# Kernel optimization log

Hardware: AMD Instinct MI355X
Metric: run time of the kernel (lower is better)

The kernel has to match this reference:

```python
import jax, jax.numpy as jnp
import numpy as np

N, Wt, Tt, DIM = 16, 256, 2048, 256
EPS = 1e-5

def silu(x):
    return x * jax.nn.sigmoid(x)

def setup_inputs() -> dict:
    key = jax.random.key(0)
    ks = jax.random.split(key, 12)
    d = {}
    d['T'] = jnp.arange(Tt, dtype=jnp.float32)
    d['durations'] = jax.random.uniform(ks[0], (N, Wt, 1), jnp.float32)
    d['features'] = jax.random.normal(ks[1], (N, Wt, DIM), jnp.float32)
    d['conv1_w'] = jax.random.normal(ks[2], (8, DIM, 3), jnp.float32) * 0.05
    d['conv1_b'] = jnp.zeros((8,), jnp.float32)
    d['bn1_g'] = jnp.ones((8,), jnp.float32)
    d['bn1_b'] = jnp.zeros((8,), jnp.float32)
    d['bn1_m'] = jnp.zeros((8,), jnp.float32)
    d['bn1_v'] = jnp.ones((8,), jnp.float32)
    d['conv2_w'] = jax.random.normal(ks[3], (8, DIM, 3), jnp.float32) * 0.05
    d['conv2_b'] = jnp.zeros((8,), jnp.float32)
    d['bn2_g'] = jnp.ones((8,), jnp.float32)
    d['bn2_b'] = jnp.zeros((8,), jnp.float32)
    d['bn2_m'] = jnp.zeros((8,), jnp.float32)
    d['bn2_v'] = jnp.ones((8,), jnp.float32)
    d['sb1_w1'] = jax.random.normal(ks[4], (10, 2), jnp.float32) * 0.3
    d['sb1_b1'] = jnp.zeros((2,), jnp.float32)
    d['sb1_w2'] = jax.random.normal(ks[5], (2, 2), jnp.float32) * 0.3
    d['sb1_b2'] = jnp.zeros((2,), jnp.float32)
    d['sb2_w1'] = jax.random.normal(ks[6], (10, 16), jnp.float32) * 0.3
    d['sb2_b1'] = jnp.zeros((16,), jnp.float32)
    d['sb2_w2'] = jax.random.normal(ks[7], (16, 16), jnp.float32) * 0.3
    d['sb2_b2'] = jnp.zeros((16,), jnp.float32)
    d['proj1_w'] = jax.random.normal(ks[8], (2, DIM), jnp.float32) * 0.3
    d['proj1_b'] = jnp.zeros((DIM,), jnp.float32)
    d['proj2_w'] = jax.random.normal(ks[9], (16, 1), jnp.float32) * 0.3
    d['proj2_b'] = jnp.zeros((1,), jnp.float32)
    return d

def _conv_bn_silu(x_ncw, w, b, g, beta, m, v):
    # Conv1d(dim->8, k=3, pad=1) + BatchNorm(eval) + SiLU
    y = jax.lax.conv_general_dilated(x_ncw, w, (1,), [(1, 1)],
                                     dimension_numbers=('NCH', 'OIH', 'NCH'))
    y = y + b[None, :, None]
    y = (y - m[None, :, None]) * jax.lax.rsqrt(v[None, :, None] + EPS)
    y = y * g[None, :, None] + beta[None, :, None]
    return silu(y)

def _swish_block(x, w1, b1, w2, b2):
    x = silu(x @ w1 + b1)
    return silu(x @ w2 + b2)

def reference(T, durations, features, conv1_w, conv1_b, bn1_g, bn1_b, bn1_m, bn1_v,
              conv2_w, conv2_b, bn2_g, bn2_b, bn2_m, bn2_v,
              sb1_w1, sb1_b1, sb1_w2, sb1_b2, sb2_w1, sb2_b1, sb2_w2, sb2_b2,
              proj1_w, proj1_b, proj2_w, proj2_b):
    feat = jnp.swapaxes(features, 1, 2)  # (N, C, W)
    n, _, w = feat.shape
    t = T.shape[0]
    left = jnp.swapaxes(_conv_bn_silu(feat, conv1_w, conv1_b, bn1_g, bn1_b, bn1_m, bn1_v), 1, 2)   # (N, W, 8)
    right = jnp.swapaxes(_conv_bn_silu(feat, conv2_w, conv2_b, bn2_g, bn2_b, bn2_m, bn2_v), 1, 2)  # (N, W, 8)
    token_end = jnp.cumsum(durations, axis=1)        # (N, W, 1)
    token_start = token_end - durations              # (N, W, 1)
    S = T[None, None, :] - token_start               # (N, W, T)
    E = token_end - T[None, None, :]                 # (N, W, T)
    left_b = jnp.broadcast_to(left[:, :, None, :], (n, w, t, 8))
    right_b = jnp.broadcast_to(right[:, :, None, :], (n, w, t, 8))
    xleft = jnp.concatenate([S[..., None], E[..., None], left_b], axis=-1)    # (N, W, T, 10)
    xright = jnp.concatenate([S[..., None], E[..., None], right_b], axis=-1)  # (N, W, T, 10)
    C = _swish_block(xleft, sb1_w1, sb1_b1, sb1_w2, sb1_b2)                   # (N, W, T, 2)
    xr = _swish_block(xright, sb2_w1, sb2_b1, sb2_w2, sb2_b2)                 # (N, W, T, 16)
    score = (xr @ proj2_w + proj2_b)[..., 0]                                  # (N, W, T)
    Wsm = jax.nn.softmax(score, axis=1)  # softmax over tokens W
    out_r = jnp.einsum('nkt,ndk->ntd', Wsm, feat)                             # (N, T, dim)
    out_l = jnp.einsum('nkt,nktp->ntp', Wsm, C) @ proj1_w + proj1_b           # (N, T, dim)
    return out_l + out_r
```

## Files before the change

kernel.cpp:

```cpp
#include <hip/hip_runtime.h>
#include <hip/hip_bf16.h>

#define NN  16
#define WT  256
#define TT  2048
#define DIM 256
#define TBT 8

typedef __attribute__((ext_vector_type(8))) short short8_t;
typedef __attribute__((ext_vector_type(4))) float f32x4;

__device__ __forceinline__ float fast_rcp(float x){ return __builtin_amdgcn_rcpf(x); }

__device__ __forceinline__ float silu_f(float x){
    return x * fast_rcp(1.0f + __expf(-x));
}

__device__ __forceinline__ unsigned short f2bf(float x){
    union { float f; unsigned u; } v; v.f = x;
    unsigned r = v.u + 0x7FFFu + ((v.u >> 16) & 1u);
    return (unsigned short)(r >> 16);
}

__device__ __forceinline__ void fma4(float4& a, float s, const float4& f){
    a.x = fmaf(s, f.x, a.x); a.y = fmaf(s, f.y, a.y);
    a.z = fmaf(s, f.z, a.z); a.w = fmaf(s, f.w, a.w);
}

__global__ __launch_bounds__(256) void prep_k(
    const float* __restrict__ dur, const float* __restrict__ feat,
    const float* __restrict__ c1w, const float* __restrict__ c1b,
    const float* __restrict__ g1,  const float* __restrict__ be1,
    const float* __restrict__ m1,  const float* __restrict__ vv1,
    const float* __restrict__ c2w, const float* __restrict__ c2b,
    const float* __restrict__ g2,  const float* __restrict__ be2,
    const float* __restrict__ m2,  const float* __restrict__ vv2,
    const float* __restrict__ sb1w1, const float* __restrict__ sb1b1,
    const float* __restrict__ sb2w1, const float* __restrict__ sb2b1,
    float* __restrict__ v1o, float* __restrict__ v2o)
{
    int w = blockIdx.x, n = blockIdx.y;
    int tid = threadIdx.x;

    __shared__ float sdur[WT];
    sdur[tid] = dur[n*WT + tid];
    __syncthreads();
    for (int off = 1; off < WT; off <<= 1){
        float v = (tid >= off) ? sdur[tid-off] : 0.0f;
        __syncthreads();
        sdur[tid] += v;
        __syncthreads();
    }
    float end   = sdur[w];
    float start = end - dur[n*WT + w];

    const float* fb = feat + (size_t)(n*WT)*DIM;
    float fm = (w > 0)    ? fb[(size_t)(w-1)*DIM + tid] : 0.0f;
    float f0 =              fb[(size_t) w   *DIM + tid];
    float fp = (w < WT-1) ? fb[(size_t)(w+1)*DIM + tid] : 0.0f;

    float pl[8], pr[8];
    #pragma unroll
    for (int o = 0; o < 8; o++){
        const float* wp = c1w + (size_t)(o*DIM + tid)*3;
        pl[o] = fmaf(fm, wp[0], fmaf(f0, wp[1], fp*wp[2]));
        const float* wq = c2w + (size_t)(o*DIM + tid)*3;
        pr[o] = fmaf(fm, wq[0], fmaf(f0, wq[1], fp*wq[2]));
    }
    #pragma unroll
    for (int o = 0; o < 8; o++){
        #pragma unroll
        for (int off = 32; off; off >>= 1){
            pl[o] += __shfl_xor(pl[o], off);
            pr[o] += __shfl_xor(pr[o], off);
        }
    }
    __shared__ float sws[4][16];
    int wave = tid >> 6, lane = tid & 63;
    if (lane == 0){
        #pragma unroll
        for (int o = 0; o < 8; o++){ sws[wave][o] = pl[o]; sws[wave][8+o] = pr[o]; }
    }
    __syncthreads();
    __shared__ float slr[16];
    if (tid < 16){
        float s = sws[0][tid] + sws[1][tid] + sws[2][tid] + sws[3][tid];
        int o = tid & 7; bool isr = tid >= 8;
        float bias = isr ? c2b[o] : c1b[o];
        float mm   = isr ? m2[o]  : m1[o];
        float vv   = isr ? vv2[o] : vv1[o];
        float gg   = isr ? g2[o]  : g1[o];
        float bb   = isr ? be2[o] : be1[o];
        float y = s + bias;
        y = (y - mm) * rsqrtf(vv + 1e-5f);
        y = y * gg + bb;
        slr[tid] = silu_f(y);
    }
    __syncthreads();
    if (tid < 16){
        int j = tid;
        float acc = sb2b1[j] - start*sb2w1[j] + end*sb2w1[16 + j];
        #pragma unroll
        for (int o = 0; o < 8; o++) acc = fmaf(slr[8+o], sb2w1[(2+o)*16 + j], acc);
        v2o[(size_t)(n*WT + w)*16 + j] = acc;
    } else if (tid < 18){
        int p = tid - 16;
        float acc = sb1b1[p] - start*sb1w1[p] + end*sb1w1[2 + p];
        #pragma unroll
        for (int o = 0; o < 8; o++) acc = fmaf(slr[o], sb1w1[(2+o)*2 + p], acc);
        v1o[(size_t)(n*WT + w)*2 + p] = acc;
    }
}

__global__ __launch_bounds__(256) void featpack_k(const float* __restrict__ feat,
                                                  unsigned short* __restrict__ featP)
{
    int kb = blockIdx.x, n = blockIdx.y;
    int d = threadIdx.x;
    const float* fb = feat + (size_t)n*WT*DIM + (size_t)kb*32*DIM + d;
    unsigned short* op = featP + ((size_t)(n*8 + kb)*DIM + d)*32;
    unsigned short buf[32];
    #pragma unroll
    for (int e = 0; e < 32; e++) buf[e] = f2bf(fb[(size_t)e*DIM]);
    #pragma unroll
    for (int g = 0; g < 4; g++){
        uint4 u;
        u.x = (unsigned)buf[g*8+0] | ((unsigned)buf[g*8+1] << 16);
        u.y = (unsigned)buf[g*8+2] | ((unsigned)buf[g*8+3] << 16);
        u.z = (unsigned)buf[g*8+4] | ((unsigned)buf[g*8+5] << 16);
        u.w = (unsigned)buf[g*8+6] | ((unsigned)buf[g*8+7] << 16);
        *(uint4*)(op + g*8) = u;
    }
}

__global__ __launch_bounds__(256) void score_k(
    const float* __restrict__ Tg,
    const float* __restrict__ v1g, const float* __restrict__ v2g,
    const float* __restrict__ sb1w1, const float* __restrict__ sb1w2, const float* __restrict__ sb1b2,
    const float* __restrict__ sb2w1, const float* __restrict__ sb2w2, const float* __restrict__ sb2b2,
    const float* __restrict__ p2w, const float* __restrict__ p2b,
    unsigned short* __restrict__ wsm_b, float* __restrict__ wc_g)
{
    int n   = blockIdx.y;
    int t0  = blockIdx.x * TBT;
    int tid = threadIdx.x;
    int w   = tid;
    int lane = tid & 63, wave = tid >> 6;

    __shared__ float s_w2[16*16];
    __shared__ float s_u2[16], s_b2[16], s_p2w[16];
    __shared__ float s_u1[2], s_w21[4], s_b21[2];
    __shared__ float s_xa[4][TBT];
    __shared__ float s_xs[4][TBT];
    __shared__ float s_xc0[4][TBT], s_xc1[4][TBT];

    s_w2[tid] = sb2w2[tid];
    if (tid < 16){
        s_u2[tid]  = sb2w1[tid] - sb2w1[16 + tid];
        s_b2[tid]  = sb2b2[tid];
        s_p2w[tid] = p2w[tid];
    } else if (tid < 18){
        int p = tid - 16;
        s_u1[p]  = sb1w1[p] - sb1w1[2 + p];
        s_b21[p] = sb1b2[p];
    } else if (tid < 22){
        s_w21[tid - 18] = sb1w2[tid - 18];
    }
    __syncthreads();

    float v2r[16];
    {
        const float4* vp = (const float4*)(v2g + (size_t)(n*WT + w)*16);
        float4 a = vp[0], b = vp[1], c = vp[2], d = vp[3];
        v2r[0]=a.x; v2r[1]=a.y; v2r[2]=a.z; v2r[3]=a.w;
        v2r[4]=b.x; v2r[5]=b.y; v2r[6]=b.z; v2r[7]=b.w;
        v2r[8]=c.x; v2r[9]=c.y; v2r[10]=c.z; v2r[11]=c.w;
        v2r[12]=d.x; v2r[13]=d.y; v2r[14]=d.z; v2r[15]=d.w;
    }
    float v1r0, v1r1;
    {
        const float* vp = v1g + (size_t)(n*WT + w)*2;
        v1r0 = vp[0]; v1r1 = vp[1];
    }
    float p2bv = p2b[0];
    float tv[TBT];
    #pragma unroll
    for (int ti = 0; ti < TBT; ti++) tv[ti] = Tg[t0 + ti];

    float scores[TBT];
    #pragma unroll
    for (int tp = 0; tp < TBT; tp += 2){
        float h2a[16], h2b[16];
        #pragma unroll
        for (int j = 0; j < 16; j++){ float b = s_b2[j]; h2a[j] = b; h2b[j] = b; }
        #pragma unroll
        for (int i = 0; i < 16; i++){
            float u = s_u2[i], v = v2r[i];
            float aa = silu_f(fmaf(tv[tp],   u, v));
            float ab = silu_f(fmaf(tv[tp+1], u, v));
            #pragma unroll
            for (int j = 0; j < 16; j++){
                float wv = s_w2[i*16 + j];
                h2a[j] = fmaf(aa, wv, h2a[j]);
                h2b[j] = fmaf(ab, wv, h2b[j]);
            }
        }
        float sa = p2bv, sb = p2bv;
        #pragma unroll
        for (int j = 0; j < 16; j++){
            float pw = s_p2w[j];
            sa = fmaf(silu_f(h2a[j]), pw, sa);
            sb = fmaf(silu_f(h2b[j]), pw, sb);
        }
        scores[tp] = sa; scores[tp+1] = sb;
    }

    float c0r[TBT], c1r[TBT];
    {
        float u10 = s_u1[0], u11 = s_u1[1];
        float w00 = s_w21[0], w01 = s_w21[1], w10 = s_w21[2], w11 = s_w21[3];
        float b0 = s_b21[0], b1 = s_b21[1];
        #pragma unroll
        for (int ti = 0; ti < TBT; ti++){
            float gl0 = silu_f(fmaf(tv[ti], u10, v1r0));
            float gl1 = silu_f(fmaf(tv[ti], u11, v1r1));
            c0r[ti] = silu_f(fmaf(gl0, w00, fmaf(gl1, w10, b0)));
            c1r[ti] = silu_f(fmaf(gl0, w01, fmaf(gl1, w11, b1)));
        }
    }

    float m[TBT];
    #pragma unroll
    for (int ti = 0; ti < TBT; ti++) m[ti] = scores[ti];
    #pragma unroll
    for (int off = 32; off; off >>= 1){
        #pragma unroll
        for (int ti = 0; ti < TBT; ti++) m[ti] = fmaxf(m[ti], __shfl_xor(m[ti], off));
    }
    if (lane == 0){
        #pragma unroll
        for (int ti = 0; ti < TBT; ti++) s_xa[wave][ti] = m[ti];
    }
    __syncthreads();
    #pragma unroll
    for (int ti = 0; ti < TBT; ti++)
        m[ti] = fmaxf(fmaxf(s_xa[0][ti], s_xa[1][ti]), fmaxf(s_xa[2][ti], s_xa[3][ti]));

    float e[TBT], ps[TBT], pc0[TBT], pc1[TBT];
    #pragma unroll
    for (int ti = 0; ti < TBT; ti++){
        e[ti]   = __expf(scores[ti] - m[ti]);
        ps[ti]  = e[ti];
        pc0[ti] = e[ti] * c0r[ti];
        pc1[ti] = e[ti] * c1r[ti];
    }
    #pragma unroll
    for (int off = 32; off; off >>= 1){
        #pragma unroll
        for (int ti = 0; ti < TBT; ti++){
            ps[ti]  += __shfl_xor(ps[ti],  off);
            pc0[ti] += __shfl_xor(pc0[ti], off);
            pc1[ti] += __shfl_xor(pc1[ti], off);
        }
    }
    if (lane == 0){
        #pragma unroll
        for (int ti = 0; ti < TBT; ti++){
            s_xs[wave][ti]  = ps[ti];
            s_xc0[wave][ti] = pc0[ti];
            s_xc1[wave][ti] = pc1[ti];
        }
    }
    __syncthreads();

    unsigned short* wbase = wsm_b + ((size_t)n*TT + t0)*WT + w;
    #pragma unroll
    for (int ti = 0; ti < TBT; ti++){
        float S  = s_xs[0][ti] + s_xs[1][ti] + s_xs[2][ti] + s_xs[3][ti];
        float rS = fast_rcp(S);
        wbase[(size_t)ti*WT] = f2bf(e[ti] * rS);
    }
    if (tid < TBT){
        int ti = tid;
        float S  = s_xs[0][ti] + s_xs[1][ti] + s_xs[2][ti] + s_xs[3][ti];
        float rS = fast_rcp(S);
        float2 wc;
        wc.x = (s_xc0[0][ti] + s_xc0[1][ti] + s_xc0[2][ti] + s_xc0[3][ti]) * rS;
        wc.y = (s_xc1[0][ti] + s_xc1[1][ti] + s_xc1[2][ti] + s_xc1[3][ti]) * rS;
        *(float2*)(wc_g + ((size_t)n*TT + t0 + ti)*2) = wc;
    }
}

__global__ __launch_bounds__(512) void outr_mfma_k(
    const unsigned short* __restrict__ wsmB, const unsigned short* __restrict__ featP,
    const float* __restrict__ wc_g,
    const float* __restrict__ p1w, const float* __restrict__ p1b,
    float* __restrict__ out)
{
    int n    = blockIdx.y;
    int t0   = blockIdx.x * 32;
    int tid  = threadIdx.x;
    int lane = tid & 63, wave = tid >> 6;
    int tw   = t0 + (wave >> 2) * 16;
    int dbase = (wave & 3) * 4;
    int l15  = lane & 15, quad = lane >> 4;

    f32x4 acc[4];
    #pragma unroll
    for (int dt = 0; dt < 4; dt++) acc[dt] = (f32x4){0.f, 0.f, 0.f, 0.f};

    const unsigned short* aPtr = wsmB + ((size_t)(n*TT + tw + l15))*WT + quad*8;

    #pragma unroll
    for (int kb = 0; kb < 8; kb++){
        short8_t af = *(const short8_t*)(aPtr + kb*32);
        const unsigned short* bp = featP + ((size_t)(n*8 + kb)*DIM + dbase*16 + l15)*32 + quad*8;
        #pragma unroll
        for (int dt = 0; dt < 4; dt++){
            short8_t bf = *(const short8_t*)(bp + (size_t)dt*16*32);
            acc[dt] = __builtin_amdgcn_mfma_f32_16x16x32_bf16(af, bf, acc[dt], 0, 0, 0);
        }
    }

    float wc0[4], wc1[4];
    #pragma unroll
    for (int r = 0; r < 4; r++){
        const float* wp = wc_g + ((size_t)(n*TT + tw + quad*4 + r))*2;
        wc0[r] = wp[0]; wc1[r] = wp[1];
    }
    float* obase = out + ((size_t)(n*TT + tw + quad*4))*DIM;
    #pragma unroll
    for (int dt = 0; dt < 4; dt++){
        int d = (dbase + dt)*16 + l15;
        float pa = p1w[d], pb2 = p1w[DIM + d], pc = p1b[d];
        #pragma unroll
        for (int r = 0; r < 4; r++){
            float val = acc[dt][r] + fmaf(wc0[r], pa, fmaf(wc1[r], pb2, pc));
            obase[(size_t)r*DIM + d] = val;
        }
    }
}

__global__ __launch_bounds__(256) void fused_k(
    const float* __restrict__ Tg, const float* __restrict__ feat,
    const float* __restrict__ v1g, const float* __restrict__ v2g,
    const float* __restrict__ sb1w1, const float* __restrict__ sb1w2, const float* __restrict__ sb1b2,
    const float* __restrict__ sb2w1, const float* __restrict__ sb2w2, const float* __restrict__ sb2b2,
    const float* __restrict__ p1w, const float* __restrict__ p1b,
    const float* __restrict__ p2w, const float* __restrict__ p2b,
    float* __restrict__ out)
{
    int n   = blockIdx.y;
    int t0  = blockIdx.x * TBT;
    int tid = threadIdx.x;
    int w   = tid;
    int lane = tid & 63, wave = tid >> 6;

    __shared__ float s_w2[16*16];
    __shared__ float s_u2[16], s_b2[16], s_p2w[16];
    __shared__ float s_u1[2], s_w21[4], s_b21[2];
    __shared__ float s_wsmT[WT][TBT];
    __shared__ float s_xa[4][TBT];
    __shared__ float s_xs[4][TBT];
    __shared__ float s_xc0[4][TBT], s_xc1[4][TBT];
    __shared__ float s_wc0[TBT], s_wc1[TBT];
    __shared__ float s_out[4][DIM];

    s_w2[tid] = sb2w2[tid];
    if (tid < 16){
        s_u2[tid]  = sb2w1[tid] - sb2w1[16 + tid];
        s_b2[tid]  = sb2b2[tid];
        s_p2w[tid] = p2w[tid];
    } else if (tid < 18){
        int p = tid - 16;
        s_u1[p]  = sb1w1[p] - sb1w1[2 + p];
        s_b21[p] = sb1b2[p];
    } else if (tid < 22){
        s_w21[tid - 18] = sb1w2[tid - 18];
    }
    __syncthreads();

    float v2r[16];
    {
        const float4* vp = (const float4*)(v2g + (size_t)(n*WT + w)*16);
        float4 a = vp[0], b = vp[1], c = vp[2], d = vp[3];
        v2r[0]=a.x; v2r[1]=a.y; v2r[2]=a.z; v2r[3]=a.w;
        v2r[4]=b.x; v2r[5]=b.y; v2r[6]=b.z; v2r[7]=b.w;
        v2r[8]=c.x; v2r[9]=c.y; v2r[10]=c.z; v2r[11]=c.w;
        v2r[12]=d.x; v2r[13]=d.y; v2r[14]=d.z; v2r[15]=d.w;
    }
    float v1r0, v1r1;
    {
        const float* vp = v1g + (size_t)(n*WT + w)*2;
        v1r0 = vp[0]; v1r1 = vp[1];
    }
    float p2bv = p2b[0];
    float tv[TBT];
    #pragma unroll
    for (int ti = 0; ti < TBT; ti++) tv[ti] = Tg[t0 + ti];

    float scores[TBT];
    #pragma unroll
    for (int tp = 0; tp < TBT; tp += 2){
        float h2a[16], h2b[16];
        #pragma unroll
        for (int j = 0; j < 16; j++){ float b = s_b2[j]; h2a[j] = b; h2b[j] = b; }
        #pragma unroll
        for (int i = 0; i < 16; i++){
            float u = s_u2[i], v = v2r[i];
            float aa = silu_f(fmaf(tv[tp],   u, v));
            float ab = silu_f(fmaf(tv[tp+1], u, v));
            #pragma unroll
            for (int j = 0; j < 16; j++){
                float wv = s_w2[i*16 + j];
                h2a[j] = fmaf(aa, wv, h2a[j]);
                h2b[j] = fmaf(ab, wv, h2b[j]);
            }
        }
        float sa = p2bv, sb = p2bv;
        #pragma unroll
        for (int j = 0; j < 16; j++){
            float pw = s_p2w[j];
            sa = fmaf(silu_f(h2a[j]), pw, sa);
            sb = fmaf(silu_f(h2b[j]), pw, sb);
        }
        scores[tp] = sa; scores[tp+1] = sb;
    }

    float c0r[TBT], c1r[TBT];
    {
        float u10 = s_u1[0], u11 = s_u1[1];
        float w00 = s_w21[0], w01 = s_w21[1], w10 = s_w21[2], w11 = s_w21[3];
        float b0 = s_b21[0], b1 = s_b21[1];
        #pragma unroll
        for (int ti = 0; ti < TBT; ti++){
            float gl0 = silu_f(fmaf(tv[ti], u10, v1r0));
            float gl1 = silu_f(fmaf(tv[ti], u11, v1r1));
            c0r[ti] = silu_f(fmaf(gl0, w00, fmaf(gl1, w10, b0)));
            c1r[ti] = silu_f(fmaf(gl0, w01, fmaf(gl1, w11, b1)));
        }
    }

    float m[TBT];
    #pragma unroll
    for (int ti = 0; ti < TBT; ti++) m[ti] = scores[ti];
    #pragma unroll
    for (int off = 32; off; off >>= 1){
        #pragma unroll
        for (int ti = 0; ti < TBT; ti++) m[ti] = fmaxf(m[ti], __shfl_xor(m[ti], off));
    }
    if (lane == 0){
        #pragma unroll
        for (int ti = 0; ti < TBT; ti++) s_xa[wave][ti] = m[ti];
    }
    __syncthreads();
    #pragma unroll
    for (int ti = 0; ti < TBT; ti++)
        m[ti] = fmaxf(fmaxf(s_xa[0][ti], s_xa[1][ti]), fmaxf(s_xa[2][ti], s_xa[3][ti]));

    float e[TBT], ps[TBT], pc0[TBT], pc1[TBT];
    #pragma unroll
    for (int ti = 0; ti < TBT; ti++){
        e[ti]  = __expf(scores[ti] - m[ti]);
        ps[ti] = e[ti];
        pc0[ti] = e[ti] * c0r[ti];
        pc1[ti] = e[ti] * c1r[ti];
    }
    #pragma unroll
    for (int off = 32; off; off >>= 1){
        #pragma unroll
        for (int ti = 0; ti < TBT; ti++){
            ps[ti]  += __shfl_xor(ps[ti],  off);
            pc0[ti] += __shfl_xor(pc0[ti], off);
            pc1[ti] += __shfl_xor(pc1[ti], off);
        }
    }
    if (lane == 0){
        #pragma unroll
        for (int ti = 0; ti < TBT; ti++){
            s_xs[wave][ti]  = ps[ti];
            s_xc0[wave][ti] = pc0[ti];
            s_xc1[wave][ti] = pc1[ti];
        }
    }
    __syncthreads();
    #pragma unroll
    for (int ti = 0; ti < TBT; ti++){
        float S  = s_xs[0][ti] + s_xs[1][ti] + s_xs[2][ti] + s_xs[3][ti];
        float rS = fast_rcp(S);
        s_wsmT[w][ti] = e[ti] * rS;
    }
    if (tid < TBT){
        int ti = tid;
        float S  = s_xs[0][ti] + s_xs[1][ti] + s_xs[2][ti] + s_xs[3][ti];
        float rS = fast_rcp(S);
        s_wc0[ti] = (s_xc0[0][ti] + s_xc0[1][ti] + s_xc0[2][ti] + s_xc0[3][ti]) * rS;
        s_wc1[ti] = (s_xc1[0][ti] + s_xc1[1][ti] + s_xc1[2][ti] + s_xc1[3][ti]) * rS;
    }
    __syncthreads();

    int wid = wave;
    int dq  = lane;
    const float* fbase = feat + (size_t)n*WT*DIM + dq*4;
    float4 acc[TBT];
    #pragma unroll
    for (int i = 0; i < TBT; i++) acc[i] = make_float4(0.f, 0.f, 0.f, 0.f);

    #pragma unroll 4
    for (int w0 = wid; w0 < WT; w0 += 4){
        float4 f = *(const float4*)(fbase + (size_t)w0*DIM);
        const float4* wp = (const float4*)&s_wsmT[w0][0];
        float4 wA = wp[0], wB = wp[1];
        fma4(acc[0], wA.x, f); fma4(acc[1], wA.y, f);
        fma4(acc[2], wA.z, f); fma4(acc[3], wA.w, f);
        fma4(acc[4], wB.x, f); fma4(acc[5], wB.y, f);
        fma4(acc[6], wB.z, f); fma4(acc[7], wB.w, f);
    }

    float pw0 = p1w[tid], pw1 = p1w[DIM + tid], pbv = p1b[tid];
    float* orow = out + ((size_t)n*TT + t0)*DIM;
    #pragma unroll
    for (int ti = 0; ti < TBT; ti++){
        __syncthreads();
        *(float4*)&s_out[wid][dq*4] = acc[ti];
        __syncthreads();
        float r = s_out[0][tid] + s_out[1][tid] + s_out[2][tid] + s_out[3][tid];
        float o = fmaf(s_wc0[ti], pw0, fmaf(s_wc1[ti], pw1, r + pbv));
        orow[(size_t)ti*DIM + tid] = o;
    }
}

extern "C" void kernel_launch(void* const* d_in, const int* in_sizes, int n_in,
                              void* d_out, int out_size, void* d_ws, size_t ws_size,
                              hipStream_t stream)
{
    const float* Tg    = (const float*)d_in[0];
    const float* dur   = (const float*)d_in[1];
    const float* feat  = (const float*)d_in[2];
    const float* c1w   = (const float*)d_in[3];
    const float* c1b   = (const float*)d_in[4];
    const float* bn1g  = (const float*)d_in[5];
    const float* bn1b  = (const float*)d_in[6];
    const float* bn1m  = (const float*)d_in[7];
    const float* bn1v  = (const float*)d_in[8];
    const float* c2w   = (const float*)d_in[9];
    const float* c2b   = (const float*)d_in[10];
    const float* bn2g  = (const float*)d_in[11];
    const float* bn2b  = (const float*)d_in[12];
    const float* bn2m  = (const float*)d_in[13];
    const float* bn2v  = (const float*)d_in[14];
    const float* sb1w1 = (const float*)d_in[15];
    const float* sb1b1 = (const float*)d_in[16];
    const float* sb1w2 = (const float*)d_in[17];
    const float* sb1b2 = (const float*)d_in[18];
    const float* sb2w1 = (const float*)d_in[19];
    const float* sb2b1 = (const float*)d_in[20];
    const float* sb2w2 = (const float*)d_in[21];
    const float* sb2b2 = (const float*)d_in[22];
    const float* p1w   = (const float*)d_in[23];
    const float* p1b   = (const float*)d_in[24];
    const float* p2w   = (const float*)d_in[25];
    const float* p2b   = (const float*)d_in[26];
    float* out = (float*)d_out;

    float* ws = (float*)d_ws;
    float* v1  = ws;
    float* v2  = ws + 8192;
    float* wc  = ws + 8192 + 65536;
    unsigned short* wsmB  = (unsigned short*)(ws + 8192 + 65536 + 65536);
    unsigned short* featP = wsmB + (size_t)NN*TT*WT;
    size_t need = ((size_t)8192 + 65536 + 65536)*sizeof(float)
                + ((size_t)NN*TT*WT + (size_t)NN*WT*DIM)*sizeof(unsigned short);

    prep_k<<<dim3(WT, NN), 256, 0, stream>>>(dur, feat, c1w, c1b, bn1g, bn1b, bn1m, bn1v,
                                             c2w, c2b, bn2g, bn2b, bn2m, bn2v,
                                             sb1w1, sb1b1, sb2w1, sb2b1, v1, v2);
    if (ws_size >= need){
        featpack_k<<<dim3(8, NN), 256, 0, stream>>>(feat, featP);
        score_k<<<dim3(TT/TBT, NN), 256, 0, stream>>>(Tg, v1, v2,
                                                      sb1w1, sb1w2, sb1b2,
                                                      sb2w1, sb2w2, sb2b2,
                                                      p2w, p2b, wsmB, wc);
        outr_mfma_k<<<dim3(TT/32, NN), 512, 0, stream>>>(wsmB, featP, wc, p1w, p1b, out);
    } else {
        fused_k<<<dim3(TT/TBT, NN), 256, 0, stream>>>(Tg, feat, v1, v2,
                                                      sb1w1, sb1w2, sb1b2,
                                                      sb2w1, sb2w2, sb2b2,
                                                      p1w, p1b, p2w, p2b, out);
    }
}
```

Baseline: 293.0 us.

## Skip saturated SiLU units in score MLP via wave-uniform linear-region detection

Result: no change. 288.0 us (-1.7%).

```diff
diff --git a/kernel.cpp b/kernel.cpp
--- a/kernel.cpp
+++ b/kernel.cpp
@@ -142,7 +142,8 @@
     unsigned short* __restrict__ wsm_b, float* __restrict__ wc_g)
 {
     int n   = blockIdx.y;
-    int t0  = blockIdx.x * TBT;
+    int bx  = (int)((blockIdx.x * 37u) & 255u);
+    int t0  = bx * TBT;
     int tid = threadIdx.x;
     int w   = tid;
     int lane = tid & 63, wave = tid >> 6;
@@ -187,32 +188,104 @@
     #pragma unroll
     for (int ti = 0; ti < TBT; ti++) tv[ti] = Tg[t0 + ti];
 
+    unsigned mpos = 0u, mneg = 0u;
+    #pragma unroll
+    for (int i = 0; i < 16; i++){
+        float u = s_u2[i], v = v2r[i];
+        float xa = fmaf(tv[0],     u, v);
+        float xb = fmaf(tv[TBT-1], u, v);
+        float lo = fminf(xa, xb), hi = fmaxf(xa, xb);
+        mpos |= ((unsigned)__all(lo >  20.0f)) << i;
+        mneg |= ((unsigned)__all(hi < -20.0f)) << i;
+    }
+    unsigned mact = 0xFFFFu & ~(mpos | mneg);
+
+    float hA[16], hB[16];
+    #pragma unroll
+    for (int j = 0; j < 16; j++){ hA[j] = s_b2[j]; hB[j] = 0.0f; }
+    #pragma unroll
+    for (int i = 0; i < 16; i++){
+        float pm = (float)((mpos >> i) & 1u);
+        float vv = v2r[i] * pm;
+        float uu = s_u2[i] * pm;
+        #pragma unroll
+        for (int j = 0; j < 16; j++){
+            float wv = s_w2[i*16 + j];
+            hA[j] = fmaf(vv, wv, hA[j]);
+            hB[j] = fmaf(uu, wv, hB[j]);
+        }
+    }
+
     float scores[TBT];
-    #pragma unroll
-    for (int tp = 0; tp < TBT; tp += 2){
-        float h2a[16], h2b[16];
-        #pragma unroll
-        for (int j = 0; j < 16; j++){ float b = s_b2[j]; h2a[j] = b; h2b[j] = b; }
-        #pragma unroll
-        for (int i = 0; i < 16; i++){
-            float u = s_u2[i], v = v2r[i];
-            float aa = silu_f(fmaf(tv[tp],   u, v));
-            float ab = silu_f(fmaf(tv[tp+1], u, v));
+    if (mact == 0u){
+        unsigned jpos = 0u, jact = 0u;
+        #pragma unroll
+        for (int j = 0; j < 16; j++){
+            float h0 = fmaf(tv[0],     hB[j], hA[j]);
+            float h7 = fmaf(tv[TBT-1], hB[j], hA[j]);
+            float lo = fminf(h0, h7), hi = fmaxf(h0, h7);
+            unsigned p  = (unsigned)__all(lo >  20.0f);
+            unsigned nn = (unsigned)__all(hi < -20.0f);
+            jpos |= p << j;
+            jact |= ((p | nn) ^ 1u) << j;
+        }
+        if (jact == 0u){
+            float SA = p2bv, SB = 0.0f;
             #pragma unroll
             for (int j = 0; j < 16; j++){
-                float wv = s_w2[i*16 + j];
-                h2a[j] = fmaf(aa, wv, h2a[j]);
-                h2b[j] = fmaf(ab, wv, h2b[j]);
+                float pw = s_p2w[j] * (float)((jpos >> j) & 1u);
+                SA = fmaf(hA[j], pw, SA);
+                SB = fmaf(hB[j], pw, SB);
             }
-        }
-        float sa = p2bv, sb = p2bv;
-        #pragma unroll
-        for (int j = 0; j < 16; j++){
-            float pw = s_p2w[j];
-            sa = fmaf(silu_f(h2a[j]), pw, sa);
-            sb = fmaf(silu_f(h2b[j]), pw, sb);
-        }
-        scores[tp] = sa; scores[tp+1] = sb;
+            #pragma unroll
+            for (int ti = 0; ti < TBT; ti++) scores[ti] = fmaf(tv[ti], SB, SA);
+        } else {
+            #pragma unroll
+            for (int ti = 0; ti < TBT; ti++){
+                float s = p2bv;
+                #pragma unroll
+                for (int j = 0; j < 16; j++){
+                    float h = fmaf(tv[ti], hB[j], hA[j]);
+                    s = fmaf(silu_f(h), s_p2w[j], s);
+                }
+                scores[ti] = s;
+            }
+        }
+    } else {
+        unsigned ms0 = (unsigned)__builtin_amdgcn_readfirstlane((int)mact);
+        const float* vrow = v2g + (size_t)(n*WT + w)*16;
+        #pragma unroll
+        for (int tp = 0; tp < TBT; tp += 2){
+            float h2a[16], h2b[16];
+            #pragma unroll
+            for (int j = 0; j < 16; j++){
+                h2a[j] = fmaf(tv[tp],   hB[j], hA[j]);
+                h2b[j] = fmaf(tv[tp+1], hB[j], hA[j]);
+            }
+            unsigned ms = ms0;
+            while (ms){
+                int i = __ffs(ms) - 1; ms &= ms - 1;
+                float u = s_u2[i];
+                float v = vrow[i];
+                float aa = silu_f(fmaf(tv[tp],   u, v));
+                float ab = silu_f(fmaf(tv[tp+1], u, v));
+                const float* wr = &s_w2[i*16];
+                #pragma unroll
+                for (int j = 0; j < 16; j++){
+                    float wv = wr[j];
+                    h2a[j] = fmaf(aa, wv, h2a[j]);
+                    h2b[j] = fmaf(ab, wv, h2b[j]);
+                }
+            }
+            float sa = p2bv, sb = p2bv;
+            #pragma unroll
+            for (int j = 0; j < 16; j++){
+                float pw = s_p2w[j];
+                sa = fmaf(silu_f(h2a[j]), pw, sa);
+                sb = fmaf(silu_f(h2b[j]), pw, sb);
+            }
+            scores[tp] = sa; scores[tp+1] = sb;
+        }
     }
 
     float c0r[TBT], c1r[TBT];
```
